# Performance work log

Hardware: AMD Instinct MI355X
Metric: run time of the kernel (lower is better)

The kernel has to match this reference:

```python
import jax, jax.numpy as jnp
import numpy as np
import math

D_MODEL = 1024
NUM_HEADS = 16
SEQ = 2048
BATCH = 4


def setup_inputs() -> dict:
    key = jax.random.key(0)
    ks = jax.random.split(key, 7)
    s = 0.02
    return {
        "x": jax.random.normal(ks[0], (BATCH, SEQ, D_MODEL), jnp.float32),
        "Wq": jax.random.normal(ks[1], (D_MODEL, D_MODEL), jnp.float32) * s,
        "bq": jax.random.normal(ks[2], (D_MODEL,), jnp.float32) * s,
        "Wkv": jax.random.normal(ks[3], (D_MODEL, 2 * D_MODEL), jnp.float32) * s,
        "bkv": jax.random.normal(ks[4], (2 * D_MODEL,), jnp.float32) * s,
        "Wo": jax.random.normal(ks[5], (D_MODEL, D_MODEL), jnp.float32) * s,
        "bo": jax.random.normal(ks[6], (D_MODEL,), jnp.float32) * s,
        "decoderMask": 1,
    }


def reference(x, Wq, bq, Wkv, bkv, Wo, bo, decoderMask):
    B, S, D = x.shape
    H = NUM_HEADS
    dh = D // H
    q_ = x @ Wq + bq              # [B,S,D]
    kv_ = x @ Wkv + bkv           # [B,S,2D] (self-attention: m is None)
    # Faithful to source: concat [q_, kv_] then reshape into heads of 3*dh,
    # which interleaves Q/KV projection columns across heads.
    qkv = jnp.concatenate([q_, kv_], axis=-1)          # [B,S,3D]
    qkv = qkv.reshape(B, S, H, 3 * dh).transpose(0, 2, 1, 3)  # [B,H,S,3dh]
    q, k, v = jnp.split(qkv, 3, axis=-1)               # each [B,H,S,dh]
    scaled = jnp.einsum("bhqd,bhkd->bhqk", q, k) / math.sqrt(dh)
    if decoderMask:
        mask = jnp.triu(jnp.full((S, S), -jnp.inf, dtype=scaled.dtype), k=1)
        scaled = scaled + mask
    attn = jax.nn.softmax(scaled, axis=-1)
    vals = jnp.einsum("bhqk,bhkd->bhqd", attn, v)      # [B,H,S,dh]
    vals = vals.transpose(0, 2, 1, 3).reshape(B, S, D)
    return vals @ Wo + bo
```

## Files before the change

kernel.cpp:

```cpp
#include <hip/hip_runtime.h>
#include <cstddef>
#include <cstdint>

#define SEQ   2048
#define BATCH 4
#define DM    1024
#define NH    16
#define DH    64
#define ROWS  (BATCH*SEQ)
#define NC3   3072
#define SM_SCALE 0.18033688f

typedef unsigned short u16;
typedef __attribute__((ext_vector_type(8))) short bf16x8;
typedef __attribute__((ext_vector_type(2))) float f32x2;
typedef __attribute__((ext_vector_type(4))) float f32x4;
typedef __attribute__((ext_vector_type(16))) float f32x16;
typedef __attribute__((ext_vector_type(4))) unsigned u32x4;
typedef __attribute__((ext_vector_type(2))) unsigned u32x2;

union V16 { f32x16 v; f32x2 p[8]; };

__device__ __forceinline__ u16 f2b(float f) {
  union { float f; unsigned u; } v; v.f = f;
  unsigned r = v.u + 0x7fffu + ((v.u >> 16) & 1u);
  return (u16)(r >> 16);
}

__device__ __forceinline__ unsigned cvt_pk_bf16(float lo, float hi) {
  unsigned r;
  asm("v_cvt_pk_bf16_f32 %0, %1, %2" : "=v"(r) : "v"(lo), "v"(hi));
  return r;
}

__device__ __forceinline__ void plswap(unsigned& a, unsigned& b) {
  auto rr = __builtin_amdgcn_permlane32_swap((int)a, (int)b, false, false);
  a = (unsigned)rr[0];
  b = (unsigned)rr[1];
}

__device__ __forceinline__ float ex2(float x) { return __builtin_amdgcn_exp2f(x); }

__device__ __forceinline__ void gld16(const void* g, void* l) {
  __builtin_amdgcn_global_load_lds((const __attribute__((address_space(1))) void*)g,
                                   (__attribute__((address_space(3))) void*)l,
                                   16, 0, 0);
}

__global__ __launch_bounds__(256) void prep_tw_kernel(
    const float* __restrict__ x, const float* __restrict__ bq,
    const float* __restrict__ bkv, u16* __restrict__ xb, float* __restrict__ bc,
    const float* __restrict__ Wq, const float* __restrict__ Wkv,
    const float* __restrict__ Wo, u16* __restrict__ Wt)
{
  __shared__ float t_[32][33];
  const int tid = threadIdx.x;
  if (blockIdx.x < 8192) {
    int i = blockIdx.x * 256 + tid;
    int idx = i * 4;
    float4 v = *(const float4*)(x + idx);
    xb[idx + 0] = f2b(v.x);
    xb[idx + 1] = f2b(v.y);
    xb[idx + 2] = f2b(v.z);
    xb[idx + 3] = f2b(v.w);
    if (i < NC3) bc[i] = (i < DM) ? bq[i] : bkv[i - DM];
  } else {
    const int bid = blockIdx.x - 8192;
    const int n0 = (bid & 127) * 32, k0 = (bid >> 7) * 32;
    const int xcol = tid & 31, yrow = tid >> 5;
    #pragma unroll
    for (int it = 0; it < 4; ++it) {
      int k = k0 + yrow + it * 8;
      int n = n0 + xcol;
      float v;
      if (n < DM)           v = Wq[k * DM + n];
      else if (n < NC3)     v = Wkv[k * (2 * DM) + (n - DM)];
      else                  v = Wo[k * DM + (n - NC3)];
      t_[yrow + it * 8][xcol] = v;
    }
    __syncthreads();
    #pragma unroll
    for (int it = 0; it < 4; ++it) {
      int n = n0 + yrow + it * 8;
      int k = k0 + xcol;
      Wt[(size_t)n * DM + k] = f2b(t_[xcol][yrow + it * 8]);
    }
  }
}

template <int MODE>
__global__ __launch_bounds__(256) void gemm_bt(
    const u16* __restrict__ A, const u16* __restrict__ Bt,
    const float* __restrict__ bias, void* __restrict__ C,
    u16* __restrict__ Vt, int M, int N, int K)
{
  __shared__ alignas(16) u16 As[2][128 * 32];
  __shared__ alignas(16) u16 Bs[2][128 * 32];
  const int tid = threadIdx.x;
  const int lane = tid & 63, wid = tid >> 6;
  const int wr = (wid >> 1) * 64, wc = (wid & 1) * 64;
  const int l15 = lane & 15, lhi = lane >> 4;
  const int row0 = blockIdx.y * 128, col0 = blockIdx.x * 128;
  const int sr = tid >> 2, scol = (tid & 3) * 8;

  f32x4 acc[4][4];
  #pragma unroll
  for (int m = 0; m < 4; ++m)
    #pragma unroll
    for (int n = 0; n < 4; ++n) { f32x4 z = {0.f, 0.f, 0.f, 0.f}; acc[m][n] = z; }

  const int KT = K >> 5;
  int cur = 0;
  gld16(A  + (size_t)(row0 + sr) * K + scol,        &As[0][sr * 32 + scol]);
  gld16(A  + (size_t)(row0 + 64 + sr) * K + scol,   &As[0][(64 + sr) * 32 + scol]);
  gld16(Bt + (size_t)(col0 + sr) * K + scol,        &Bs[0][sr * 32 + scol]);
  gld16(Bt + (size_t)(col0 + 64 + sr) * K + scol,   &Bs[0][(64 + sr) * 32 + scol]);

  for (int kt = 0; kt < KT; ++kt) {
    __syncthreads();
    if (kt + 1 < KT) {
      const int k1 = (kt + 1) << 5;
      const int nb = cur ^ 1;
      gld16(A  + (size_t)(row0 + sr) * K + k1 + scol,      &As[nb][sr * 32 + scol]);
      gld16(A  + (size_t)(row0 + 64 + sr) * K + k1 + scol, &As[nb][(64 + sr) * 32 + scol]);
      gld16(Bt + (size_t)(col0 + sr) * K + k1 + scol,      &Bs[nb][sr * 32 + scol]);
      gld16(Bt + (size_t)(col0 + 64 + sr) * K + k1 + scol, &Bs[nb][(64 + sr) * 32 + scol]);
    }
    bf16x8 a[4], bfr[4];
    #pragma unroll
    for (int m = 0; m < 4; ++m)
      a[m] = *(const bf16x8*)&As[cur][(wr + m * 16 + l15) * 32 + lhi * 8];
    #pragma unroll
    for (int n = 0; n < 4; ++n)
      bfr[n] = *(const bf16x8*)&Bs[cur][(wc + n * 16 + l15) * 32 + lhi * 8];
    #pragma unroll
    for (int m = 0; m < 4; ++m)
      #pragma unroll
      for (int n = 0; n < 4; ++n)
        acc[m][n] = __builtin_amdgcn_mfma_f32_16x16x32_bf16(a[m], bfr[n], acc[m][n], 0, 0, 0);
    cur ^= 1;
  }

  #pragma unroll
  for (int m = 0; m < 4; ++m)
    #pragma unroll
    for (int n = 0; n < 4; ++n) {
      const int col = col0 + wc + n * 16 + l15;
      const float bv = bias[col];
      if (MODE == 0) {
        #pragma unroll
        for (int r = 0; r < 4; ++r) {
          const int row = row0 + wr + m * 16 + lhi * 4 + r;
          ((float*)C)[(size_t)row * N + col] = acc[m][n][r] + bv;
        }
      } else {
        const int hh = col / 192;
        const int cc = col - hh * 192;
        const float qs = (cc < 64) ? SM_SCALE : 1.f;
        u16 wv[4];
        #pragma unroll
        for (int r = 0; r < 4; ++r) {
          const int row = row0 + wr + m * 16 + lhi * 4 + r;
          wv[r] = f2b((acc[m][n][r] + bv) * qs);
          ((u16*)C)[(size_t)row * N + col] = wv[r];
        }
        if (cc >= 128) {
          const int row = row0 + wr + m * 16 + lhi * 4;
          const int bb = row >> 11, j = row & (SEQ - 1);
          u16* vt = Vt + ((size_t)(bb * NH + hh) * 64 + (cc - 128)) * SEQ + j;
          u32x2 pv = { (unsigned)wv[0] | ((unsigned)wv[1] << 16),
                       (unsigned)wv[2] | ((unsigned)wv[3] << 16) };
          *(u32x2*)vt = pv;
        }
      }
    }
}

__global__ __launch_bounds__(256) void attn_kernel(
    const u16* __restrict__ qkv, const u16* __restrict__ Vt, u16* __restrict__ ctx)
{
  const int bid = blockIdx.x;
  const int p   = (bid >> 3) & 7;
  const int g   = (bid & 7) + ((bid >> 6) << 3);
  const int h   = g & 15, b = g >> 4;
  const int tid = threadIdx.x;
  const int lane = tid & 63, wid = tid >> 6;
  const int l31 = lane & 31, lhi5 = lane >> 5;

  __shared__ alignas(16) u16 smem[4 * 64 * 64];

  const size_t kv_row = (size_t)(b * NH + h) * 64;
  const int sr = tid >> 3, sck = tid & 7;
  const int scks = sck ^ (sr & 7);

  const u16* kSrc0 = qkv + (size_t)(b * SEQ + sr) * NC3 + h * 192 + 64 + scks * 8;
  const u16* kSrc1 = kSrc0 + (size_t)32 * NC3;
  const u16* vSrc0 = Vt + (kv_row + sr) * SEQ + scks * 8;
  const u16* vSrc1 = vSrc0 + (size_t)32 * SEQ;
  const int dOff0 = sr * 64 + sck * 8;
  const int dOff1 = (32 + sr) * 64 + sck * 8;

  int koff[4], koff2[4];
  #pragma unroll
  for (int c = 0; c < 4; ++c) {
    koff[c]  = l31 * 64        + (((2 * c + lhi5) ^ (l31 & 7)) * 8);
    koff2[c] = (32 + l31) * 64 + (((2 * c + lhi5) ^ (l31 & 7)) * 8);
  }

  #pragma unroll 1
  for (int half = 0; half < 2; ++half) {
    const int qt = half ? (7 - p) : (8 + p);
    const int q0 = qt * 128;

    #pragma unroll
    for (int it = 0; it < 4; ++it) {
      int row = it * 32 + sr;
      gld16(qkv + (size_t)(b * SEQ + q0 + row) * NC3 + h * 192 + scks * 8,
            &smem[row * 64 + sck * 8]);
    }
    gld16(kSrc0, &smem[8192 + dOff0]);
    gld16(kSrc1, &smem[8192 + dOff1]);
    gld16(vSrc0, &smem[12288 + dOff0]);
    gld16(vSrc1, &smem[12288 + dOff1]);
    __syncthreads();

    bf16x8 qf[4];
    {
      const int qrow = wid * 32 + l31;
      #pragma unroll
      for (int c = 0; c < 4; ++c)
        qf[c] = *(const bf16x8*)&smem[qrow * 64 + (((2 * c + lhi5) ^ (qrow & 7)) * 8)];
    }
    __syncthreads();

    V16 o0, o1;
    #pragma unroll
    for (int r = 0; r < 16; ++r) { o0.v[r] = 0.f; o1.v[r] = 0.f; }
    float lrow = 0.f;

    const int nt = qt * 2 + 2;
    const int qw0 = q0 + wid * 32;
    const int qa  = qw0 + l31;
    const int dqb = qa - 4 * lhi5;

    for (int jt = 0; jt < nt; ++jt) {
      const int j0 = jt * 64;
      const u16* Kb = smem + ((jt & 1) ? 0 : 8192);
      const u16* Vb = smem + ((jt & 1) ? 4096 : 12288);

      if (jt + 1 < nt) {
        u16* Kn = smem + ((jt & 1) ? 8192 : 0);
        u16* Vn = smem + ((jt & 1) ? 12288 : 4096);
        const size_t kAdv = (size_t)(j0 + 64) * NC3;
        const int    vAdv = j0 + 64;
        gld16(kSrc0 + kAdv, &Kn[dOff0]);
        gld16(kSrc1 + kAdv, &Kn[dOff1]);
        gld16(vSrc0 + vAdv, &Vn[dOff0]);
        gld16(vSrc1 + vAdv, &Vn[dOff1]);
      }

      if (j0 <= qw0 + 31) {
        V16 s0, s1;
        #pragma unroll
        for (int r = 0; r < 16; ++r) { s0.v[r] = 0.f; s1.v[r] = 0.f; }
        __builtin_amdgcn_s_setprio(1);
        #pragma unroll
        for (int c = 0; c < 4; ++c) {
          bf16x8 kf = *(const bf16x8*)&Kb[koff[c]];
          s0.v = __builtin_amdgcn_mfma_f32_32x32x16_bf16(kf, qf[c], s0.v, 0, 0, 0);
        }
        #pragma unroll
        for (int c = 0; c < 4; ++c) {
          bf16x8 kf = *(const bf16x8*)&Kb[koff2[c]];
          s1.v = __builtin_amdgcn_mfma_f32_32x32x16_bf16(kf, qf[c], s1.v, 0, 0, 0);
        }
        __builtin_amdgcn_s_setprio(0);

        if (j0 + 63 > qw0) {
          const int dq = dqb - j0;
          #pragma unroll
          for (int r = 0; r < 16; ++r) {
            const int kvc = (r & 3) + 8 * (r >> 2);
            s0.v[r] = (kvc > dq)      ? -1e30f : s0.v[r];
            s1.v[r] = (kvc + 32 > dq) ? -1e30f : s1.v[r];
          }
        }

        f32x2 sum2 = {0.f, 0.f};
        #pragma unroll
        for (int i = 0; i < 8; ++i) {
          f32x2 e0, e1;
          e0[0] = ex2(s0.p[i][0]); e0[1] = ex2(s0.p[i][1]);
          e1[0] = ex2(s1.p[i][0]); e1[1] = ex2(s1.p[i][1]);
          s0.p[i] = e0; s1.p[i] = e1;
          sum2 += e0 + e1;
        }
        float ps = sum2[0] + sum2[1];
        {
          unsigned a = __builtin_bit_cast(unsigned, ps), bb = a;
          plswap(a, bb);
          ps = __builtin_bit_cast(float, a) + __builtin_bit_cast(float, bb);
        }
        lrow += ps;

        unsigned pk0[8], pk1[8];
        #pragma unroll
        for (int i = 0; i < 4; ++i) {
          pk0[2 * i]     = cvt_pk_bf16(s0.v[4 * i + 0], s0.v[4 * i + 1]);
          pk0[2 * i + 1] = cvt_pk_bf16(s0.v[4 * i + 2], s0.v[4 * i + 3]);
          pk1[2 * i]     = cvt_pk_bf16(s1.v[4 * i + 0], s1.v[4 * i + 1]);
          pk1[2 * i + 1] = cvt_pk_bf16(s1.v[4 * i + 2], s1.v[4 * i + 3]);
        }
        bf16x8 pf[4];
        {
          unsigned a0 = pk0[0], b0 = pk0[2]; plswap(a0, b0);
          unsigned a1 = pk0[1], b1 = pk0[3]; plswap(a1, b1);
          u32x4 w0v = {a0, a1, b0, b1}; pf[0] = __builtin_bit_cast(bf16x8, w0v);
          unsigned a2 = pk0[4], b2 = pk0[6]; plswap(a2, b2);
          unsigned a3 = pk0[5], b3 = pk0[7]; plswap(a3, b3);
          u32x4 w1v = {a2, a3, b2, b3}; pf[1] = __builtin_bit_cast(bf16x8, w1v);
          unsigned a4 = pk1[0], b4 = pk1[2]; plswap(a4, b4);
          unsigned a5 = pk1[1], b5 = pk1[3]; plswap(a5, b5);
          u32x4 w2v = {a4, a5, b4, b5}; pf[2] = __builtin_bit_cast(bf16x8, w2v);
          unsigned a6 = pk1[4], b6 = pk1[6]; plswap(a6, b6);
          unsigned a7 = pk1[5], b7 = pk1[7]; plswap(a7, b7);
          u32x4 w3v = {a6, a7, b6, b7}; pf[3] = __builtin_bit_cast(bf16x8, w3v);
        }

        __builtin_amdgcn_s_setprio(1);
        #pragma unroll
        for (int c = 0; c < 4; ++c) {
          bf16x8 vf = *(const bf16x8*)&Vb[koff[c]];
          o0.v = __builtin_amdgcn_mfma_f32_32x32x16_bf16(vf, pf[c], o0.v, 0, 0, 0);
        }
        #pragma unroll
        for (int c = 0; c < 4; ++c) {
          bf16x8 vf = *(const bf16x8*)&Vb[koff2[c]];
          o1.v = __builtin_amdgcn_mfma_f32_32x32x16_bf16(vf, pf[c], o1.v, 0, 0, 0);
        }
        __builtin_amdgcn_s_setprio(0);
      }
      __syncthreads();
    }

    const float inv = 1.f / lrow;
    u16* crow = ctx + (size_t)(b * SEQ + qa) * DM + h * DH;
    #pragma unroll
    for (int i = 0; i < 4; ++i) {
      u32x2 v0, v1;
      v0[0] = cvt_pk_bf16(o0.v[4 * i + 0] * inv, o0.v[4 * i + 1] * inv);
      v0[1] = cvt_pk_bf16(o0.v[4 * i + 2] * inv, o0.v[4 * i + 3] * inv);
      v1[0] = cvt_pk_bf16(o1.v[4 * i + 0] * inv, o1.v[4 * i + 1] * inv);
      v1[1] = cvt_pk_bf16(o1.v[4 * i + 2] * inv, o1.v[4 * i + 3] * inv);
      *(u32x2*)&crow[8 * i + 4 * lhi5]      = v0;
      *(u32x2*)&crow[32 + 8 * i + 4 * lhi5] = v1;
    }
  }
}

extern "C" void kernel_launch(void* const* d_in, const int* in_sizes, int n_in,
                              void* d_out, int out_size, void* d_ws, size_t ws_size,
                              hipStream_t stream) {
  (void)in_sizes; (void)n_in; (void)out_size; (void)ws_size;
  const float* x   = (const float*)d_in[0];
  const float* Wq  = (const float*)d_in[1];
  const float* bq  = (const float*)d_in[2];
  const float* Wkv = (const float*)d_in[3];
  const float* bkv = (const float*)d_in[4];
  const float* Wo  = (const float*)d_in[5];
  const float* bo  = (const float*)d_in[6];
  float* out = (float*)d_out;

  char* w = (char*)d_ws;
  size_t off = 0;
  auto alloc = [&](size_t bytes) { void* p = w + off; off += (bytes + 255) & ~(size_t)255; return p; };
  u16*   xb   = (u16*)alloc((size_t)ROWS * DM * 2);
  u16*   qkvb = (u16*)alloc((size_t)ROWS * NC3 * 2);
  u16*   Vt   = (u16*)alloc((size_t)BATCH * NH * DH * SEQ * 2);
  u16*   Wt   = (u16*)alloc((size_t)4096 * DM * 2);
  float* bc   = (float*)alloc((size_t)NC3 * 4);
  u16*   ctx  = xb;

  prep_tw_kernel<<<dim3(8192 + 4096), 256, 0, stream>>>(x, bq, bkv, xb, bc, Wq, Wkv, Wo, Wt);
  gemm_bt<1><<<dim3(NC3 / 128, ROWS / 128), 256, 0, stream>>>(xb, Wt, bc, qkvb, Vt, ROWS, NC3, DM);
  attn_kernel<<<dim3(512), 256, 0, stream>>>(qkvb, Vt, ctx);
  gemm_bt<0><<<dim3(DM / 128, ROWS / 128), 256, 0, stream>>>(ctx, Wt + (size_t)NC3 * DM, bo, out, nullptr, ROWS, DM, DM);
}
```

Baseline: 172.5 us.

## Deepen GEMM global-to-LDS pipeline to four stages with explicit vmcnt waits

```diff
diff --git a/kernel.cpp b/kernel.cpp
--- a/kernel.cpp
+++ b/kernel.cpp
@@ -94,8 +94,7 @@
     const float* __restrict__ bias, void* __restrict__ C,
     u16* __restrict__ Vt, int M, int N, int K)
 {
-  __shared__ alignas(16) u16 As[2][128 * 32];
-  __shared__ alignas(16) u16 Bs[2][128 * 32];
+  __shared__ alignas(16) u16 lds_[4 * 8192];
   const int tid = threadIdx.x;
   const int lane = tid & 63, wid = tid >> 6;
   const int wr = (wid >> 1) * 64, wc = (wid & 1) * 64;
@@ -103,6 +102,18 @@
   const int row0 = blockIdx.y * 128, col0 = blockIdx.x * 128;
   const int sr = tid >> 2, scol = (tid & 3) * 8;
 
+  const u16* aS0 = A  + (size_t)(row0 + sr) * K + scol;
+  const u16* aS1 = A  + (size_t)(row0 + 64 + sr) * K + scol;
+  const u16* bS0 = Bt + (size_t)(col0 + sr) * K + scol;
+  const u16* bS1 = Bt + (size_t)(col0 + 64 + sr) * K + scol;
+  const int dA = tid * 8;
+
+  int aoff[4], boff[4];
+  #pragma unroll
+  for (int m = 0; m < 4; ++m) aoff[m] = (wr + m * 16 + l15) * 32 + lhi * 8;
+  #pragma unroll
+  for (int n = 0; n < 4; ++n) boff[n] = 4096 + (wc + n * 16 + l15) * 32 + lhi * 8;
+
   f32x4 acc[4][4];
   #pragma unroll
   for (int m = 0; m < 4; ++m)
@@ -110,35 +121,39 @@
     for (int n = 0; n < 4; ++n) { f32x4 z = {0.f, 0.f, 0.f, 0.f}; acc[m][n] = z; }
 
   const int KT = K >> 5;
-  int cur = 0;
-  gld16(A  + (size_t)(row0 + sr) * K + scol,        &As[0][sr * 32 + scol]);
-  gld16(A  + (size_t)(row0 + 64 + sr) * K + scol,   &As[0][(64 + sr) * 32 + scol]);
-  gld16(Bt + (size_t)(col0 + sr) * K + scol,        &Bs[0][sr * 32 + scol]);
-  gld16(Bt + (size_t)(col0 + 64 + sr) * K + scol,   &Bs[0][(64 + sr) * 32 + scol]);
+
+  auto stage = [&](int kt) {
+    u16* base = lds_ + (kt & 3) * 8192;
+    const int ka = kt * 32;
+    gld16(aS0 + ka, base + dA);
+    gld16(aS1 + ka, base + 2048 + dA);
+    gld16(bS0 + ka, base + 4096 + dA);
+    gld16(bS1 + ka, base + 6144 + dA);
+  };
+
+  stage(0); stage(1); stage(2);
+  asm volatile("s_waitcnt vmcnt(8)" ::: "memory");
+  __builtin_amdgcn_s_barrier();
 
   for (int kt = 0; kt < KT; ++kt) {
-    __syncthreads();
-    if (kt + 1 < KT) {
-      const int k1 = (kt + 1) << 5;
-      const int nb = cur ^ 1;
-      gld16(A  + (size_t)(row0 + sr) * K + k1 + scol,      &As[nb][sr * 32 + scol]);
-      gld16(A  + (size_t)(row0 + 64 + sr) * K + k1 + scol, &As[nb][(64 + sr) * 32 + scol]);
-      gld16(Bt + (size_t)(col0 + sr) * K + k1 + scol,      &Bs[nb][sr * 32 + scol]);
-      gld16(Bt + (size_t)(col0 + 64 + sr) * K + k1 + scol, &Bs[nb][(64 + sr) * 32 + scol]);
-    }
-    bf16x8 a[4], bfr[4];
-    #pragma unroll
-    for (int m = 0; m < 4; ++m)
-      a[m] = *(const bf16x8*)&As[cur][(wr + m * 16 + l15) * 32 + lhi * 8];
-    #pragma unroll
-    for (int n = 0; n < 4; ++n)
-      bfr[n] = *(const bf16x8*)&Bs[cur][(wc + n * 16 + l15) * 32 + lhi * 8];
+    const u16* buf = lds_ + (kt & 3) * 8192;
+    bf16x8 a[4], b[4];
+    #pragma unroll
+    for (int m = 0; m < 4; ++m) a[m] = *(const bf16x8*)&buf[aoff[m]];
+    #pragma unroll
+    for (int n = 0; n < 4; ++n) b[n] = *(const bf16x8*)&buf[boff[n]];
+    if (kt + 3 < KT) stage(kt + 3);
+    __builtin_amdgcn_s_setprio(1);
     #pragma unroll
     for (int m = 0; m < 4; ++m)
       #pragma unroll
       for (int n = 0; n < 4; ++n)
-        acc[m][n] = __builtin_amdgcn_mfma_f32_16x16x32_bf16(a[m], bfr[n], acc[m][n], 0, 0, 0);
-    cur ^= 1;
+        acc[m][n] = __builtin_amdgcn_mfma_f32_16x16x32_bf16(a[m], b[n], acc[m][n], 0, 0, 0);
+    __builtin_amdgcn_s_setprio(0);
+    if (kt + 3 < KT)      { asm volatile("s_waitcnt vmcnt(8)" ::: "memory"); }
+    else if (kt + 2 < KT) { asm volatile("s_waitcnt vmcnt(4)" ::: "memory"); }
+    else if (kt + 1 < KT) { asm volatile("s_waitcnt vmcnt(0)" ::: "memory"); }
+    __builtin_amdgcn_s_barrier();
   }
 
   #pragma unroll
```

Result: faster. 167.5 us (-2.9%).
